# Performance work log

Hardware: AMD Instinct MI355X
Metric: run time of the kernel (lower is better)

The kernel has to match this reference:

```python
import jax, jax.numpy as jnp
import numpy as np

# dims
B, DM, H, W = 2, 768, 64, 64   # d_model = in_chans*patch^2 = 48*16
EXPAND, DSTATE, DCONV = 2, 4, 3
DI = DM * EXPAND               # 1536
R = DM // 16                   # dt_rank = 48


def setup_inputs() -> dict:
    key = jax.random.key(0)
    ks = jax.random.split(key, 8)
    s = 0.02
    # dt bias init (softplus-inverse of dt ~ LogUniform[1e-3, 1e-1])
    dt = jnp.exp(jax.random.uniform(ks[5], (1, DI)) * (np.log(0.1) - np.log(0.001)) + np.log(0.001))
    dt = jnp.clip(dt, 1e-4)
    inv_dt = dt + jnp.log(-jnp.expm1(-dt))
    A_log = jnp.log(jnp.arange(1, DSTATE + 1, dtype=jnp.float32))  # (n,)
    A_log = jnp.broadcast_to(A_log[None, None, :], (1, DI, DSTATE))
    return {
        "hidden_states": jax.random.normal(ks[0], (B, DM, H, W), jnp.float32),
        "in_proj_w": jax.random.normal(ks[1], (DI, DM), jnp.float32) * s,
        "conv_w": jax.random.normal(ks[2], (DI, 1, DCONV, DCONV), jnp.float32) * s,  # depthwise OIHW
        "conv_b": jnp.zeros((DI,), jnp.float32),
        "x_proj_w": jax.random.normal(ks[3], (R + 2 * DSTATE, DI), jnp.float32) * s,
        "dt_w": jax.random.uniform(ks[4], (1, DI, R), jnp.float32, -(R ** -0.5), R ** -0.5),
        "dt_b": inv_dt,
        "A_log": A_log,
        "D_param": jnp.ones((1, DI), jnp.float32),
        "ln_g": jnp.ones((DI,), jnp.float32),
        "ln_b": jnp.zeros((DI,), jnp.float32),
        "out_proj_w": jax.random.normal(ks[6], (DM, DI), jnp.float32) * s,
    }


def reference(hidden_states, in_proj_w, conv_w, conv_b, x_proj_w, dt_w, dt_b,
              A_log, D_param, ln_g, ln_b, out_proj_w):
    b, dm, h, w = hidden_states.shape
    L = h * w
    hs = jnp.transpose(hidden_states, (0, 2, 3, 1))          # b h w dm
    x = hs @ in_proj_w.T                                     # b h w di
    xs = jnp.transpose(x, (0, 3, 1, 2))                      # b di h w
    pad = (DCONV - 1) // 2
    xs = jax.lax.conv_general_dilated(
        xs, conv_w, (1, 1), ((pad, pad), (pad, pad)),
        feature_group_count=xs.shape[1],
        dimension_numbers=("NCHW", "OIHW", "NCHW")) + conv_b[None, :, None, None]
    xs = xs * jax.nn.sigmoid(xs)                             # SiLU
    xs_seq = jnp.transpose(xs, (0, 2, 3, 1)).reshape(b, L, -1)  # b l di

    x_dbl = xs_seq @ x_proj_w.T                              # b l (R+2N)
    dt, Bs, Cs = jnp.split(x_dbl, [R, R + DSTATE], axis=-1)  # b l R / b l n / b l n
    delta = jnp.einsum("blr,dr->bdl", dt, dt_w[0])           # b di l
    delta = jax.nn.softplus(delta + dt_b[0][None, :, None])  # delta_softplus + bias
    u = jnp.transpose(xs_seq, (0, 2, 1))                     # b di l

    A = -jnp.exp(A_log[0])                                   # di n
    dA = jnp.exp(delta[..., None] * A[None, :, None, :])     # b di l n
    dBu = (delta * u)[..., None] * Bs[:, None, :, :]         # b di l n

    def comb(e1, e2):
        a1, x1 = e1
        a2, x2 = e2
        return a2 * a1, a2 * x1 + x2

    _, states = jax.lax.associative_scan(comb, (dA, dBu), axis=2)  # b di l n
    y = jnp.einsum("bdln,bln->bdl", states, Cs) + D_param[0][None, :, None] * u
    y = jnp.transpose(y, (0, 2, 1))                          # b l di

    mu = y.mean(-1, keepdims=True)
    var = y.var(-1, keepdims=True)
    y = (y - mu) * jax.lax.rsqrt(var + 1e-5) * ln_g + ln_b    # LayerNorm

    y = y.reshape(b, h, w, -1)
    out = y @ out_proj_w.T                                   # b h w dm
    return jnp.transpose(out, (0, 3, 1, 2))                  # b dm h w
```

## Files before the change

### kernel.cpp

```cpp
#include <hip/hip_runtime.h>
#include <math.h>

#define B_   2
#define DM_  768
#define L_   4096
#define DI_  1536
#define NS_  4
#define R_   48
#define XD_  56

typedef __attribute__((ext_vector_type(8))) short s16x8;
typedef __attribute__((ext_vector_type(4))) float f32x4;
typedef __attribute__((ext_vector_type(8))) unsigned short us8;
typedef __attribute__((ext_vector_type(4))) unsigned short us4;

__device__ __forceinline__ float softplus_f(float x) {
    return fmaxf(x, 0.f) + log1pf(expf(-fabsf(x)));
}
__device__ __forceinline__ float silu_f(float x) {
    return x / (1.f + expf(-x));
}

__device__ __forceinline__ unsigned short bf16_rn(float v) {
    unsigned u = __float_as_uint(v);
    u += 0x7FFFu + ((u >> 16) & 1u);
    return (unsigned short)(u >> 16);
}
__device__ __forceinline__ void split2(float v, unsigned short& h, unsigned short& l) {
    h = bf16_rn(v);
    float fh = __uint_as_float(((unsigned)h) << 16);
    l = bf16_rn(v - fh);
}

__device__ __forceinline__ void cp16(const void* g, void* l) {
    __builtin_amdgcn_global_load_lds(
        (const __attribute__((address_space(1))) unsigned int*)g,
        (__attribute__((address_space(3))) unsigned int*)l, 16, 0, 0);
}

__global__ __launch_bounds__(256) void split_w(const float* __restrict__ W,
    unsigned short* __restrict__ Wh, unsigned short* __restrict__ Wl, int n4)
{
    int id = blockIdx.x * 256 + threadIdx.x;
    if (id >= n4) return;
    float4 v = *(const float4*)(W + (size_t)id * 4);
    us4 h, l;
    unsigned short hh, ll;
    split2(v.x, hh, ll); h[0] = hh; l[0] = ll;
    split2(v.y, hh, ll); h[1] = hh; l[1] = ll;
    split2(v.z, hh, ll); h[2] = hh; l[2] = ll;
    split2(v.w, hh, ll); h[3] = hh; l[3] = ll;
    *(us4*)(Wh + (size_t)id * 4) = h;
    *(us4*)(Wl + (size_t)id * 4) = l;
}

template<int K, bool LN>
__global__ __launch_bounds__(256) void pack_x(
    const float* __restrict__ X,
    unsigned short* __restrict__ Xh, unsigned short* __restrict__ Xl,
    const float* __restrict__ mu, const float* __restrict__ rs,
    const float* __restrict__ g, const float* __restrict__ be)
{
    const int KT = K / 32;
    int kt = blockIdx.x, lt = blockIdx.y, b = blockIdx.z;
    __shared__ float t[32][133];
    int tid = threadIdx.x;
    const float* Xp = X + ((size_t)b * K + kt * 32) * L_ + lt * 128;
#pragma unroll
    for (int i = 0; i < 4; ++i) {
        int id = i * 256 + tid;
        int k = id >> 5, f4 = id & 31;
        float4 v = *(const float4*)(Xp + (size_t)k * L_ + f4 * 4);
        t[k][f4 * 4]     = v.x;
        t[k][f4 * 4 + 1] = v.y;
        t[k][f4 * 4 + 2] = v.z;
        t[k][f4 * 4 + 3] = v.w;
    }
    __syncthreads();
    size_t tb = ((size_t)(b * 32 + lt) * KT + kt) * 5120;
    unsigned short* ph = Xh + tb;
    unsigned short* pl = Xl + tb;
#pragma unroll
    for (int i = 0; i < 2; ++i) {
        int id = i * 256 + tid;
        int l = id >> 2, kbv = id & 3;
        float m = 0.f, r = 1.f;
        if (LN) { m = mu[b * L_ + lt * 128 + l]; r = rs[b * L_ + lt * 128 + l]; }
        us8 hv, lv;
#pragma unroll
        for (int j = 0; j < 8; ++j) {
            int k = kbv * 8 + j;
            float v = t[k][l];
            if (LN) v = (v - m) * r * g[kt * 32 + k] + be[kt * 32 + k];
            unsigned short hh, ll;
            split2(v, hh, ll);
            hv[j] = hh; lv[j] = ll;
        }
        *(us8*)(ph + l * 40 + kbv * 8) = hv;
        *(us8*)(pl + l * 40 + kbv * 8) = lv;
    }
}

template<int K, int MBF>
__global__ __launch_bounds__(256) void gemm_mfma(
    const unsigned short* __restrict__ Wh, const unsigned short* __restrict__ Wl,
    const unsigned short* __restrict__ Xh, const unsigned short* __restrict__ Xl,
    float* __restrict__ C, int N)
{
    const int KT = K / 32;
    const int BN = MBF * 32;
    __shared__ unsigned short lds[10240];
    int tid = threadIdx.x;
    int lt = blockIdx.x, nt = blockIdx.y, b = blockIdx.z;
    int lane = tid & 63, w = tid >> 6;
    int wn = (w >> 1) * (MBF * 16), wl = (w & 1) * 64;
    int row = lane & 15, kb = lane >> 4;

    const unsigned short* xh_t = Xh + ((size_t)(b * 32 + lt) * KT) * 5120;
    const unsigned short* xl_t = Xl + ((size_t)(b * 32 + lt) * KT) * 5120;
    const unsigned short* wh_p = Wh + (size_t)(nt * BN + wn + row) * K + kb * 8;
    const unsigned short* wl_p = Wl + (size_t)(nt * BN + wn + row) * K + kb * 8;

    f32x4 acc[MBF][4];
#pragma unroll
    for (int m = 0; m < MBF; m++)
#pragma unroll
        for (int l2 = 0; l2 < 4; l2++) acc[m][l2] = (f32x4){0.f, 0.f, 0.f, 0.f};

    for (int kt = 0; kt < KT; ++kt) {
        const unsigned short* sh = xh_t + (size_t)kt * 5120;
        const unsigned short* sl = xl_t + (size_t)kt * 5120;
#pragma unroll
        for (int i = 0; i < 3; ++i) {
            int slot = i * 256 + tid;
            if (slot < 640) {
                int lbase = (i * 256 + (tid & 192)) * 8;
                cp16(sh + slot * 8, &lds[lbase]);
                cp16(sl + slot * 8, &lds[5120 + lbase]);
            }
        }
        s16x8 ah[MBF], al[MBF];
#pragma unroll
        for (int m = 0; m < MBF; m++) {
            ah[m] = *(const s16x8*)(wh_p + (size_t)m * 16 * K + kt * 32);
            al[m] = *(const s16x8*)(wl_p + (size_t)m * 16 * K + kt * 32);
        }
        __syncthreads();
        s16x8 bh[4], bl[4];
#pragma unroll
        for (int l2 = 0; l2 < 4; l2++) {
            int off = (wl + l2 * 16 + row) * 40 + kb * 8;
            bh[l2] = *(const s16x8*)&lds[off];
            bl[l2] = *(const s16x8*)&lds[5120 + off];
        }
#pragma unroll
        for (int m = 0; m < MBF; m++)
#pragma unroll
            for (int l2 = 0; l2 < 4; l2++) {
                acc[m][l2] = __builtin_amdgcn_mfma_f32_16x16x32_bf16(ah[m], bh[l2], acc[m][l2], 0, 0, 0);
                acc[m][l2] = __builtin_amdgcn_mfma_f32_16x16x32_bf16(ah[m], bl[l2], acc[m][l2], 0, 0, 0);
                acc[m][l2] = __builtin_amdgcn_mfma_f32_16x16x32_bf16(al[m], bh[l2], acc[m][l2], 0, 0, 0);
            }
        __syncthreads();
    }
    float* Cp = C + ((size_t)b * N + nt * BN) * L_ + (size_t)lt * 128;
#pragma unroll
    for (int m = 0; m < MBF; m++)
#pragma unroll
        for (int l2 = 0; l2 < 4; l2++) {
            int lcol = wl + l2 * 16 + row;
#pragma unroll
            for (int j = 0; j < 4; j++) {
                int nrow = wn + m * 16 + kb * 4 + j;
                Cp[(size_t)nrow * L_ + lcol] = acc[m][l2][j];
            }
        }
}

template<int K, int N, int ACT>
__global__ __launch_bounds__(256) void gemm64(
    const float* __restrict__ A, int aBatch,
    const float* __restrict__ Wm,
    float* __restrict__ C,
    const float* __restrict__ bias)
{
    const int L = L_;
    __shared__ float As[16][64];
    __shared__ float Ws[16][68];
    int tid = threadIdx.x;
    int b  = blockIdx.z;
    int l0 = blockIdx.x * 64;
    int n0 = blockIdx.y * 64;
    const float* Ab = A + (size_t)b * aBatch;
    float acc[4][4];
#pragma unroll
    for (int j = 0; j < 4; j++)
#pragma unroll
        for (int i = 0; i < 4; i++) acc[j][i] = 0.f;
    int tl = tid & 15, tn = tid >> 4;

    for (int k0 = 0; k0 < K; k0 += 16) {
#pragma unroll
        for (int i = 0; i < 4; i++) {
            int idx = i * 256 + tid;
            int k = idx >> 6, l = idx & 63;
            As[k][l] = Ab[(size_t)(k0 + k) * L + l0 + l];
        }
#pragma unroll
        for (int i = 0; i < 4; i++) {
            int idx = i * 256 + tid;
            int n = idx >> 4, k = idx & 15;
            float v = 0.f;
            if (N % 64 == 0 || n0 + n < N)
                v = Wm[(size_t)(n0 + n) * K + k0 + k];
            Ws[k][n] = v;
        }
        __syncthreads();
#pragma unroll
        for (int k = 0; k < 16; k++) {
            float4 a4 = *(const float4*)&As[k][tl * 4];
            float4 w4 = *(const float4*)&Ws[k][tn * 4];
            float av[4] = {a4.x, a4.y, a4.z, a4.w};
            float wv[4] = {w4.x, w4.y, w4.z, w4.w};
#pragma unroll
            for (int j = 0; j < 4; j++)
#pragma unroll
                for (int i = 0; i < 4; i++)
                    acc[j][i] += wv[j] * av[i];
        }
        __syncthreads();
    }
#pragma unroll
    for (int j = 0; j < 4; j++) {
        int n = n0 + tn * 4 + j;
        if (N % 64 != 0 && n >= N) continue;
        float bsn = (ACT == 1) ? bias[n] : 0.f;
        float4 o;
        float* po = &o.x;
#pragma unroll
        for (int i = 0; i < 4; i++) {
            float v = acc[j][i];
            if (ACT == 1) v = softplus_f(v + bsn);
            po[i] = v;
        }
        *(float4*)&C[((size_t)b * N + n) * L + l0 + tl * 4] = o;
    }
}

__global__ __launch_bounds__(256) void conv_silu(
    const float* __restrict__ x, const float* __restrict__ wc,
    const float* __restrict__ bias, float* __restrict__ u)
{
    int d = blockIdx.x, b = blockIdx.y;
    __shared__ float t[66 * 66];
    const float* xp = x + ((size_t)b * DI_ + d) * (size_t)L_;
    int tid = threadIdx.x;
    for (int idx = tid; idx < 66 * 66; idx += 256) {
        int r = idx / 66, c = idx - r * 66;
        int h = r - 1, w2 = c - 1;
        float v = 0.f;
        if (h >= 0 && h < 64 && w2 >= 0 && w2 < 64) v = xp[h * 64 + w2];
        t[idx] = v;
    }
    __syncthreads();
    float w9[9];
#pragma unroll
    for (int i = 0; i < 9; i++) w9[i] = wc[d * 9 + i];
    float bi = bias[d];
    float* up = u + ((size_t)b * DI_ + d) * (size_t)L_;
#pragma unroll
    for (int it = 0; it < 16; it++) {
        int p = it * 256 + tid;
        int h = p >> 6, c = p & 63;
        float s = 0.f;
#pragma unroll
        for (int kh = 0; kh < 3; kh++)
#pragma unroll
            for (int kw = 0; kw < 3; kw++)
                s += t[(h + kh) * 66 + (c + kw)] * w9[kh * 3 + kw];
        s += bi;
        up[p] = silu_f(s);
    }
}

__global__ __launch_bounds__(256) void scan_kernel(
    float* __restrict__ dly,
    const float* __restrict__ u,
    const float* __restrict__ xdbl,
    const float* __restrict__ A_log,
    const float* __restrict__ Dp)
{
    const int L = L_;
    int d = blockIdx.x, b = blockIdx.y;
    int tid = threadIdx.x;
    int lane = tid & 63, wv = tid >> 6;
    size_t rowoff = ((size_t)b * DI_ + d) * (size_t)L + tid * 16;
    float dl[16], uu[16];
#pragma unroll
    for (int i = 0; i < 4; i++) {
        *(float4*)&dl[i * 4] = *(const float4*)&dly[rowoff + i * 4];
        *(float4*)&uu[i * 4] = *(const float4*)&u[rowoff + i * 4];
    }
    float An[4];
#pragma unroll
    for (int n = 0; n < 4; n++) An[n] = -expf(A_log[d * 4 + n]);
    float Dd = Dp[d];
    const float* xb = xdbl + (size_t)b * XD_ * L + tid * 16;

    float la[4], ls[4];
#pragma unroll
    for (int n = 0; n < 4; n++) {
        float Bv[16];
#pragma unroll
        for (int i = 0; i < 4; i++)
            *(float4*)&Bv[i * 4] = *(const float4*)&xb[(size_t)(R_ + n) * L + i * 4];
        float aa = 1.f, ss = 0.f;
#pragma unroll
        for (int i = 0; i < 16; i++) {
            float ai = expf(dl[i] * An[n]);
            ss = ai * ss + dl[i] * uu[i] * Bv[i];
            aa *= ai;
        }
        la[n] = aa; ls[n] = ss;
    }
#pragma unroll
    for (int off = 1; off < 64; off <<= 1) {
#pragma unroll
        for (int n = 0; n < 4; n++) {
            float pa = __shfl_up(la[n], off);
            float ps = __shfl_up(ls[n], off);
            if (lane >= off) {
                ls[n] = ls[n] + la[n] * ps;
                la[n] = la[n] * pa;
            }
        }
    }
    float ea[4], es[4];
#pragma unroll
    for (int n = 0; n < 4; n++) {
        ea[n] = __shfl_up(la[n], 1);
        es[n] = __shfl_up(ls[n], 1);
        if (lane == 0) { ea[n] = 1.f; es[n] = 0.f; }
    }
    __shared__ float wsum[4][8];
    if (lane == 63) {
#pragma unroll
        for (int n = 0; n < 4; n++) { wsum[wv][n] = la[n]; wsum[wv][4 + n] = ls[n]; }
    }
    __syncthreads();
    float carry[4];
#pragma unroll
    for (int n = 0; n < 4; n++) {
        float wss = 0.f;
        for (int w2 = 0; w2 < wv; w2++) {
            float a2 = wsum[w2][n], s2 = wsum[w2][4 + n];
            wss = a2 * wss + s2;
        }
        carry[n] = ea[n] * wss + es[n];
    }
    float yv[16];
#pragma unroll
    for (int i = 0; i < 16; i++) yv[i] = Dd * uu[i];
#pragma unroll
    for (int n = 0; n < 4; n++) {
        float Bv[16], Cv[16];
#pragma unroll
        for (int i = 0; i < 4; i++) {
            *(float4*)&Bv[i * 4] = *(const float4*)&xb[(size_t)(R_ + n) * L + i * 4];
            *(float4*)&Cv[i * 4] = *(const float4*)&xb[(size_t)(R_ + 4 + n) * L + i * 4];
        }
        float s = carry[n];
#pragma unroll
        for (int i = 0; i < 16; i++) {
            float ai = expf(dl[i] * An[n]);
            s = ai * s + dl[i] * uu[i] * Bv[i];
            yv[i] += s * Cv[i];
        }
    }
#pragma unroll
    for (int i = 0; i < 4; i++)
        *(float4*)&dly[rowoff + i * 4] = *(const float4*)&yv[i * 4];
}

__global__ __launch_bounds__(256) void ln_stats(
    const float* __restrict__ y, float* __restrict__ mu, float* __restrict__ rs)
{
    int tid = threadIdx.x;
    int lsub = tid & 31, dg = tid >> 5;
    int l = blockIdx.x * 32 + lsub;
    int b = blockIdx.y;
    const float* yp = y + (size_t)b * DI_ * L_ + l;
    float s = 0.f, s2 = 0.f;
    for (int d = dg; d < DI_; d += 8) {
        float v = yp[(size_t)d * L_];
        s += v; s2 += v * v;
    }
    __shared__ float sh[2][8][32];
    sh[0][dg][lsub] = s; sh[1][dg][lsub] = s2;
    __syncthreads();
    if (dg == 0) {
#pragma unroll
        for (int g2 = 1; g2 < 8; g2++) { s += sh[0][g2][lsub]; s2 += sh[1][g2][lsub]; }
        const float inv = 1.f / DI_;
        float m = s * inv;
        float var = s2 * inv - m * m;
        mu[b * L_ + l] = m;
        rs[b * L_ + l] = rsqrtf(var + 1e-5f);
    }
}

extern "C" void kernel_launch(void* const* d_in, const int* in_sizes, int n_in,
                              void* d_out, int out_size, void* d_ws, size_t ws_size,
                              hipStream_t stream)
{
    const float* hidden = (const float*)d_in[0];
    const float* in_w   = (const float*)d_in[1];
    const float* conv_w = (const float*)d_in[2];
    const float* conv_b = (const float*)d_in[3];
    const float* xp_w   = (const float*)d_in[4];
    const float* dt_w   = (const float*)d_in[5];
    const float* dt_b   = (const float*)d_in[6];
    const float* A_log  = (const float*)d_in[7];
    const float* Dp     = (const float*)d_in[8];
    const float* ln_g   = (const float*)d_in[9];
    const float* ln_b   = (const float*)d_in[10];
    const float* out_w  = (const float*)d_in[11];
    float* out = (float*)d_out;

    const size_t BIG = (size_t)B_ * DI_ * L_;
    float* big1 = (float*)d_ws;
    float* big2 = big1 + BIG;
    float* xdbl = big2 + BIG;
    float* mu   = xdbl + (size_t)B_ * XD_ * L_;
    float* rs   = mu + (size_t)B_ * L_;
    unsigned short* pack = (unsigned short*)(rs + (size_t)B_ * L_);

    const size_t NK = (size_t)DI_ * DM_;
    const size_t XPK = (size_t)B_ * 32 * (DM_ / 32) * 5120;
    const size_t YPK = (size_t)B_ * 32 * (DI_ / 32) * 5120;
    unsigned short* wh = pack;
    unsigned short* wlo = pack + NK;
    unsigned short* xh = pack + 2 * NK;

    split_w<<<(int)(NK / 4 / 256), 256, 0, stream>>>(in_w, wh, wlo, (int)(NK / 4));
    pack_x<DM_, false><<<dim3(DM_ / 32, 32, B_), 256, 0, stream>>>(
        hidden, xh, xh + XPK, nullptr, nullptr, nullptr, nullptr);
    gemm_mfma<DM_, 4><<<dim3(32, DI_ / 128, B_), 256, 0, stream>>>(
        wh, wlo, xh, xh + XPK, big1, DI_);

    conv_silu<<<dim3(DI_, B_), 256, 0, stream>>>(big1, conv_w, conv_b, big2);
    gemm64<DI_, XD_, 0><<<dim3(L_ / 64, 1, B_), 256, 0, stream>>>(
        big2, DI_ * L_, xp_w, xdbl, nullptr);
    gemm64<R_, DI_, 1><<<dim3(L_ / 64, DI_ / 64, B_), 256, 0, stream>>>(
        xdbl, XD_ * L_, dt_w, big1, dt_b);
    scan_kernel<<<dim3(DI_, B_), 256, 0, stream>>>(big1, big2, xdbl, A_log, Dp);
    ln_stats<<<dim3(L_ / 32, B_), 256, 0, stream>>>(big1, mu, rs);

    split_w<<<(int)(NK / 4 / 256), 256, 0, stream>>>(out_w, wh, wlo, (int)(NK / 4));
    unsigned short* yh = pack + 2 * NK;
    pack_x<DI_, true><<<dim3(DI_ / 32, 32, B_), 256, 0, stream>>>(
        big1, yh, yh + YPK, mu, rs, ln_g, ln_b);
    gemm_mfma<DI_, 2><<<dim3(32, DM_ / 64, B_), 256, 0, stream>>>(
        wh, wlo, yh, yh + YPK, out, DM_);
}
```

Baseline: 673.7 us.

## Split-K the x_proj GEMM and swizzle MFMA GEMM workgroup order

The x_proj GEMM (N=56, K=1536) previously ran on only 128 workgroups. It now splits K into 12 chunks, giving 1536 workgroups that write partial sums, followed by a reduction kernel. This targets the GPU being underfilled during that stage, at the cost of extra partial-buffer traffic and one more launch. The MFMA GEMMs also remap block IDs with an XCD-style swizzle so neighbouring tiles land on the same chiplet, which should improve L2 reuse.

```diff
diff --git a/kernel.cpp b/kernel.cpp
--- a/kernel.cpp
+++ b/kernel.cpp
@@ -8,6 +8,9 @@
 #define NS_  4
 #define R_   48
 #define XD_  56
+
+#define KSX_  12
+#define KCHX_ 128
 
 typedef __attribute__((ext_vector_type(8))) short s16x8;
 typedef __attribute__((ext_vector_type(4))) float f32x4;
@@ -111,7 +114,14 @@
     const int BN = MBF * 32;
     __shared__ unsigned short lds[10240];
     int tid = threadIdx.x;
-    int lt = blockIdx.x, nt = blockIdx.y, b = blockIdx.z;
+    int NT = gridDim.y;
+    int nwg = 32 * NT * (int)gridDim.z;
+    int bid = blockIdx.x + 32 * (blockIdx.y + NT * blockIdx.z);
+    int cpx = nwg >> 3;
+    int swz = (bid & 7) * cpx + (bid >> 3);
+    int nt = swz % NT; int t2 = swz / NT;
+    int lt = t2 & 31;  int b  = t2 >> 5;
+
     int lane = tid & 63, w = tid >> 6;
     int wn = (w >> 1) * (MBF * 16), wl = (w & 1) * 64;
     int row = lane & 15, kb = lane >> 4;
@@ -175,6 +185,81 @@
                 Cp[(size_t)nrow * L_ + lcol] = acc[m][l2][j];
             }
         }
+}
+
+__global__ __launch_bounds__(256) void xproj_sk(
+    const float* __restrict__ u, const float* __restrict__ Wm,
+    float* __restrict__ part)
+{
+    __shared__ float As[16][64];
+    __shared__ float Ws[16][68];
+    int tid = threadIdx.x;
+    int l0 = blockIdx.x * 64;
+    int ks = blockIdx.y;
+    int b  = blockIdx.z;
+    int kbase = ks * KCHX_;
+    const float* Ab = u + (size_t)b * DI_ * L_;
+    float acc[4][4];
+#pragma unroll
+    for (int j = 0; j < 4; j++)
+#pragma unroll
+        for (int i = 0; i < 4; i++) acc[j][i] = 0.f;
+    int tl = tid & 15, tn = tid >> 4;
+
+    for (int k0 = 0; k0 < KCHX_; k0 += 16) {
+#pragma unroll
+        for (int i = 0; i < 4; i++) {
+            int idx = i * 256 + tid;
+            int k = idx >> 6, l = idx & 63;
+            As[k][l] = Ab[(size_t)(kbase + k0 + k) * L_ + l0 + l];
+        }
+#pragma unroll
+        for (int i = 0; i < 4; i++) {
+            int idx = i * 256 + tid;
+            int n = idx >> 4, k = idx & 15;
+            float v = 0.f;
+            if (n < XD_) v = Wm[(size_t)n * DI_ + kbase + k0 + k];
+            Ws[k][n] = v;
+        }
+        __syncthreads();
+#pragma unroll
+        for (int k = 0; k < 16; k++) {
+            float4 a4 = *(const float4*)&As[k][tl * 4];
+            float4 w4 = *(const float4*)&Ws[k][tn * 4];
+            float av[4] = {a4.x, a4.y, a4.z, a4.w};
+            float wv[4] = {w4.x, w4.y, w4.z, w4.w};
+#pragma unroll
+            for (int j = 0; j < 4; j++)
+#pragma unroll
+                for (int i = 0; i < 4; i++)
+                    acc[j][i] += wv[j] * av[i];
+        }
+        __syncthreads();
+    }
+#pragma unroll
+    for (int j = 0; j < 4; j++) {
+        int n = tn * 4 + j;
+        if (n >= XD_) continue;
+        float4 o = {acc[j][0], acc[j][1], acc[j][2], acc[j][3]};
+        *(float4*)&part[(((size_t)b * KSX_ + ks) * XD_ + n) * L_ + l0 + tl * 4] = o;
+    }
+}
+
+__global__ __launch_bounds__(256) void xproj_reduce(
+    const float* __restrict__ part, float* __restrict__ xdbl)
+{
+    const int tot = B_ * XD_ * L_ / 4;
+    int id = blockIdx.x * 256 + threadIdx.x;
+    if (id >= tot) return;
+    int per_b = XD_ * L_ / 4;
+    int b = id / per_b, rem = id - b * per_b;
+    float4 s = {0.f, 0.f, 0.f, 0.f};
+#pragma unroll
+    for (int ks = 0; ks < KSX_; ks++) {
+        float4 v = *(const float4*)&part[((size_t)(b * KSX_ + ks) * XD_) * L_ + (size_t)rem * 4];
+        s.x += v.x; s.y += v.y; s.z += v.z; s.w += v.w;
+    }
+    *(float4*)&xdbl[(size_t)b * XD_ * L_ + (size_t)rem * 4] = s;
 }
 
 template<int K, int N, int ACT>
@@ -441,6 +526,7 @@
     unsigned short* wh = pack;
     unsigned short* wlo = pack + NK;
     unsigned short* xh = pack + 2 * NK;
+    float* xpart = (float*)(pack + 2 * NK);
 
     split_w<<<(int)(NK / 4 / 256), 256, 0, stream>>>(in_w, wh, wlo, (int)(NK / 4));
     pack_x<DM_, false><<<dim3(DM_ / 32, 32, B_), 256, 0, stream>>>(
@@ -449,8 +535,8 @@
         wh, wlo, xh, xh + XPK, big1, DI_);
 
     conv_silu<<<dim3(DI_, B_), 256, 0, stream>>>(big1, conv_w, conv_b, big2);
-    gemm64<DI_, XD_, 0><<<dim3(L_ / 64, 1, B_), 256, 0, stream>>>(
-        big2, DI_ * L_, xp_w, xdbl, nullptr);
+    xproj_sk<<<dim3(L_ / 64, KSX_, B_), 256, 0, stream>>>(big2, xp_w, xpart);
+    xproj_reduce<<<(B_ * XD_ * L_ / 4 + 255) / 256, 256, 0, stream>>>(xpart, xdbl);
     gemm64<R_, DI_, 1><<<dim3(L_ / 64, DI_ / 64, B_), 256, 0, stream>>>(
         xdbl, XD_ * L_, dt_w, big1, dt_b);
     scan_kernel<<<dim3(DI_, B_), 256, 0, stream>>>(big1, big2, xdbl, A_log, Dp);
```

Result: faster. 555.4 us (-17.6%).
